# Kernel tuning notes

Measured on AMD Instinct MI355X. Metric: run time of the kernel, lower is better.

Reference implementation:

```python
import jax, jax.numpy as jnp
import numpy as np

H = 256; W = 256; N = 512
TANFOVX = 0.5; TANFOVY = 0.5
FX = W / (2.0 * TANFOVX)   # focal_x
FY = H / (2.0 * TANFOVY)   # focal_y


def _quat_to_rot(q):
    # q: [N,4] (w,x,y,z), normalized inside
    q = q / jnp.linalg.norm(q, axis=-1, keepdims=True)
    r, x, y, z = q[:, 0], q[:, 1], q[:, 2], q[:, 3]
    R = jnp.stack([
        1 - 2 * (y * y + z * z), 2 * (x * y - r * z), 2 * (x * z + r * y),
        2 * (x * y + r * z), 1 - 2 * (x * x + z * z), 2 * (y * z - r * x),
        2 * (x * z - r * y), 2 * (y * z + r * x), 1 - 2 * (x * x + y * y)],
        axis=-1).reshape(-1, 3, 3)
    return R


def _camera():
    # row-vector convention: t = [p,1] @ V ; full proj = V @ Pclip (3DGS style)
    V = np.eye(4, dtype=np.float32)
    V[3, :3] = [0.0, 0.0, 5.0]            # camera 5 units back along -z
    zn, zf = 0.01, 100.0
    P = np.zeros((4, 4), np.float32)
    P[0, 0] = 1.0 / TANFOVX
    P[1, 1] = 1.0 / TANFOVY
    P[2, 2] = zf / (zf - zn)
    P[3, 2] = -zf * zn / (zf - zn)
    P[2, 3] = 1.0
    return jnp.asarray(V), jnp.asarray(V @ P)


def setup_inputs() -> dict:
    key = jax.random.key(0)
    ks = jax.random.split(key, 5)
    means3D = jax.random.normal(ks[0], (N, 3), jnp.float32)
    opacities = jax.random.uniform(ks[1], (N, 1), jnp.float32)
    colors_precomp = jax.random.uniform(ks[2], (N, 3), jnp.float32)
    scales = 0.05 * jax.random.uniform(ks[3], (N, 3), jnp.float32) + 0.01
    rotations = jax.random.normal(ks[4], (N, 4), jnp.float32)
    viewmatrix, projmatrix = _camera()
    return dict(means3D=means3D, opacities=opacities,
                colors_precomp=colors_precomp, scales=scales,
                rotations=rotations, bg=jnp.zeros((3,), jnp.float32),
                viewmatrix=viewmatrix, projmatrix=projmatrix,
                campos=jnp.array([0.0, 0.0, -5.0], jnp.float32))


def _rasterize(means3D, opacities, colors, scales, rotations, bg,
               viewmatrix, projmatrix):
    n = means3D.shape[0]
    # --- 3D covariance: Sigma = (R S)(R S)^T ---
    Rm = _quat_to_rot(rotations)
    M = Rm * scales[:, None, :]                       # [N,3,3]
    Sigma = jnp.einsum('nij,nkj->nik', M, M)
    # --- camera-space positions ---
    ph = jnp.concatenate([means3D, jnp.ones((n, 1), means3D.dtype)], axis=1)
    t = ph @ viewmatrix                               # [N,4]
    tz = t[:, 2]
    tzc = jnp.maximum(tz, 1e-4)
    limx, limy = 1.3 * TANFOVX, 1.3 * TANFOVY
    txc = jnp.clip(t[:, 0] / tzc, -limx, limx) * tzc
    tyc = jnp.clip(t[:, 1] / tzc, -limy, limy) * tzc
    # --- EWA 2D covariance ---
    z0 = jnp.zeros_like(tz)
    J = jnp.stack([
        jnp.stack([FX / tzc, z0, -FX * txc / (tzc * tzc)], axis=-1),
        jnp.stack([z0, FY / tzc, -FY * tyc / (tzc * tzc)], axis=-1)],
        axis=1)                                        # [N,2,3]
    Wc = viewmatrix[:3, :3].T                          # column-vector rotation
    T = jnp.einsum('nij,jk->nik', J, Wc)               # [N,2,3]
    cov2d = jnp.einsum('nij,njk,nlk->nil', T, Sigma, T)
    cov2d = cov2d + 0.3 * jnp.eye(2, dtype=cov2d.dtype)  # low-pass dilation
    c00, c01, c11 = cov2d[:, 0, 0], cov2d[:, 0, 1], cov2d[:, 1, 1]
    det = c00 * c11 - c01 * c01
    det_inv = 1.0 / jnp.where(det != 0, det, 1.0)
    A = c11 * det_inv; B = -c01 * det_inv; C = c00 * det_inv  # conic
    mid = 0.5 * (c00 + c11)
    lam = mid + jnp.sqrt(jnp.maximum(mid * mid - det, 0.1))
    visible = (det > 0) & (tz > 0.2)
    radii = jnp.where(visible, jnp.ceil(3.0 * jnp.sqrt(lam)), 0.0).astype(jnp.int32)
    # --- screen-space means (ndc2pix) ---
    phom = ph @ projmatrix
    pw = 1.0 / (phom[:, 3] + 1e-7)
    mx = ((phom[:, 0] * pw + 1.0) * W - 1.0) * 0.5
    my = ((phom[:, 1] * pw + 1.0) * H - 1.0) * 0.5
    # --- depth sort (front-to-back) ---
    order = jnp.argsort(tz)
    mx, my = mx[order], my[order]
    A_, B_, C_ = A[order], B[order], C[order]
    op = opacities[order, 0]
    vis = visible[order]
    cols = colors[order]
    zs = tz[order]
    # --- per-pixel Gaussian evaluation [P, N] ---
    xs = jnp.arange(W, dtype=means3D.dtype)
    ys = jnp.arange(H, dtype=means3D.dtype)
    pix_x = jnp.tile(xs, H)
    pix_y = jnp.repeat(ys, W)
    dx = mx[None, :] - pix_x[:, None]
    dy = my[None, :] - pix_y[:, None]
    power = -0.5 * (A_[None, :] * dx * dx + C_[None, :] * dy * dy) \
            - B_[None, :] * dx * dy
    alpha = jnp.minimum(0.99, op[None, :] * jnp.exp(power))
    valid = (power <= 0.0) & vis[None, :] & (alpha >= 1.0 / 255.0)
    alpha = jnp.where(valid, alpha, 0.0)
    # --- front-to-back alpha compositing ---
    cum = jnp.cumprod(1.0 - alpha, axis=1)
    Tprev = jnp.concatenate(
        [jnp.ones((alpha.shape[0], 1), alpha.dtype), cum[:, :-1]], axis=1)
    wgt = alpha * Tprev                               # [P,N]
    Tfinal = cum[:, -1]
    color = wgt @ cols + Tfinal[:, None] * bg[None, :]
    depth = wgt @ zs
    color = color.reshape(H, W, 3).transpose(2, 0, 1)  # [3,H,W]
    return color, depth.reshape(H, W), Tfinal.reshape(H, W), radii


def reference(means3D, opacities, colors_precomp, scales, rotations, bg,
              viewmatrix, projmatrix, campos):
    return _rasterize(means3D, opacities, colors_precomp, scales, rotations,
                      bg, viewmatrix, projmatrix)
```

## Files before the change

kernel.cpp:

```cpp
#include <hip/hip_runtime.h>
#include <hip/hip_fp16.h>
#include <math.h>

#define NG 512
#define WI 256
#define HI 256
#define FXc 256.0f
#define FYc 256.0f
#define P2MIN -7.9943534368588578f

#if __has_builtin(__builtin_amdgcn_exp2f)
#define EXP2F(x) __builtin_amdgcn_exp2f(x)
#else
#define EXP2F(x) exp2f(x)
#endif

__global__ __launch_bounds__(256) void gs_fused(
    const float* __restrict__ means,
    const float* __restrict__ opac,
    const float* __restrict__ cols,
    const float* __restrict__ scales,
    const float* __restrict__ rots,
    const float* __restrict__ Vm,
    const float* __restrict__ Pm,
    const float* __restrict__ bg,
    float* __restrict__ out)
{
    __shared__ __align__(16) float4 us[NG*2];
    __shared__ __align__(16) float4 cs[NG*2];
    __shared__ float skey[NG];
    __shared__ int wtot[4];

    int tx   = threadIdx.x;
    int lane = tx & 63;
    int wv   = tx >> 6;
    int y    = blockIdx.x;
    float yf = (float)y;

    float4 q0r[2], q1r[2];
    float tzs[2], myv[2], ycl[2], radf[2];

    #pragma unroll
    for (int i = 0; i < 2; ++i) {
        int g = 2*tx + i;

        float qr = rots[g*4+0], qx = rots[g*4+1], qy = rots[g*4+2], qz = rots[g*4+3];
        float inv = rsqrtf(qr*qr + qx*qx + qy*qy + qz*qz);
        qr *= inv; qx *= inv; qy *= inv; qz *= inv;
        float R00 = 1.f - 2.f*(qy*qy + qz*qz);
        float R01 = 2.f*(qx*qy - qr*qz);
        float R02 = 2.f*(qx*qz + qr*qy);
        float R10 = 2.f*(qx*qy + qr*qz);
        float R11 = 1.f - 2.f*(qx*qx + qz*qz);
        float R12 = 2.f*(qy*qz - qr*qx);
        float R20 = 2.f*(qx*qz - qr*qy);
        float R21 = 2.f*(qy*qz + qr*qx);
        float R22 = 1.f - 2.f*(qx*qx + qy*qy);

        float s0 = scales[g*3+0], s1 = scales[g*3+1], s2 = scales[g*3+2];
        float M00=R00*s0, M01=R01*s1, M02=R02*s2;
        float M10=R10*s0, M11=R11*s1, M12=R12*s2;
        float M20=R20*s0, M21=R21*s1, M22=R22*s2;

        float S00 = M00*M00 + M01*M01 + M02*M02;
        float S01 = M00*M10 + M01*M11 + M02*M12;
        float S02 = M00*M20 + M01*M21 + M02*M22;
        float S11 = M10*M10 + M11*M11 + M12*M12;
        float S12 = M10*M20 + M11*M21 + M12*M22;
        float S22 = M20*M20 + M21*M21 + M22*M22;

        float px = means[g*3+0], py = means[g*3+1], pz = means[g*3+2];
        float t0 = px*Vm[0] + py*Vm[4] + pz*Vm[8]  + Vm[12];
        float t1 = px*Vm[1] + py*Vm[5] + pz*Vm[9]  + Vm[13];
        float tz = px*Vm[2] + py*Vm[6] + pz*Vm[10] + Vm[14];
        float tzc = fmaxf(tz, 1e-4f);
        const float limx = 1.3f*0.5f, limy = 1.3f*0.5f;
        float txc = fminf(fmaxf(t0 / tzc, -limx), limx) * tzc;
        float tyc = fminf(fmaxf(t1 / tzc, -limy), limy) * tzc;

        float J00 = FXc / tzc;
        float J02 = -FXc * txc / (tzc * tzc);
        float J11 = FYc / tzc;
        float J12 = -FYc * tyc / (tzc * tzc);

        float Ta0 = J00*Vm[0] + J02*Vm[2];
        float Ta1 = J00*Vm[4] + J02*Vm[6];
        float Ta2 = J00*Vm[8] + J02*Vm[10];
        float Tb0 = J11*Vm[1] + J12*Vm[2];
        float Tb1 = J11*Vm[5] + J12*Vm[6];
        float Tb2 = J11*Vm[9] + J12*Vm[10];

        float u0 = Ta0*S00 + Ta1*S01 + Ta2*S02;
        float u1 = Ta0*S01 + Ta1*S11 + Ta2*S12;
        float u2 = Ta0*S02 + Ta1*S12 + Ta2*S22;
        float v0 = Tb0*S00 + Tb1*S01 + Tb2*S02;
        float v1 = Tb0*S01 + Tb1*S11 + Tb2*S12;
        float v2 = Tb0*S02 + Tb1*S12 + Tb2*S22;
        float c00 = u0*Ta0 + u1*Ta1 + u2*Ta2 + 0.3f;
        float c01 = u0*Tb0 + u1*Tb1 + u2*Tb2;
        float c11 = v0*Tb0 + v1*Tb1 + v2*Tb2 + 0.3f;

        float det = c00*c11 - c01*c01;
        float det_inv = 1.f / ((det != 0.f) ? det : 1.f);
        float Aa =  c11 * det_inv;
        float Bb = -c01 * det_inv;
        float Cc =  c00 * det_inv;

        float mid = 0.5f*(c00 + c11);
        float lam = mid + sqrtf(fmaxf(mid*mid - det, 0.1f));
        bool vis = (det > 0.f) && (tz > 0.2f);
        radf[i] = vis ? ceilf(3.f*sqrtf(lam)) : 0.f;

        float h0 = px*Pm[0] + py*Pm[4] + pz*Pm[8]  + Pm[12];
        float h1 = px*Pm[1] + py*Pm[5] + pz*Pm[9]  + Pm[13];
        float h3 = px*Pm[3] + py*Pm[7] + pz*Pm[11] + Pm[15];
        float pw = 1.f / (h3 + 1e-7f);
        float mx = ((h0*pw + 1.f)*WI - 1.f)*0.5f;
        float my = ((h1*pw + 1.f)*HI - 1.f)*0.5f;

        float opv = vis ? opac[g] : 0.f;

        const float L2E = 1.4426950408889634f;
        float A2 = -0.5f*L2E*Aa;
        float B2 = -L2E*Bb;
        float C2 = -0.5f*L2E*Cc;
        float lop = (opv > 0.f) ? log2f(opv) : -3.0e38f;

        float a  = 0.5f*L2E*Aa;
        float c  = 0.5f*L2E*Cc;
        float b  = L2E*Bb;
        float qmax  = lop + 7.9943534368588578f;
        float cmarg = c - b*b/(4.f*a);
        float amarg = a - b*b/(4.f*c);
        float dxmin = fmaxf(0.f, fmaxf(-mx, mx - 255.f));
        bool alive = vis && (opv > 0.f) && (qmax >= 0.f) && (cmarg > 0.f)
                     && (amarg*dxmin*dxmin <= qmax);
        ycl[i] = alive ? sqrtf(qmax/cmarg) + 0.0625f : -1.f;

        union { __half2 h; float f; } prg, pbt;
        prg.h = __halves2half2(__float2half_rn(cols[g*3+0]), __float2half_rn(cols[g*3+1]));
        pbt.h = __halves2half2(__float2half_rn(cols[g*3+2]), __float2half_rn(tz));

        q0r[i] = make_float4(mx, my, A2, B2);
        q1r[i] = make_float4(C2, lop, prg.f, pbt.f);
        tzs[i] = tz;
        myv[i] = my;
    }

    if (y == 0) {
        float* radii_out = out + 5*WI*HI;
        radii_out[2*tx]   = radf[0];
        radii_out[2*tx+1] = radf[1];
    }

    bool f0 = fabsf(myv[0] - yf) <= ycl[0];
    bool f1 = fabsf(myv[1] - yf) <= ycl[1];

    unsigned long long m0 = __ballot(f0);
    unsigned long long m1 = __ballot(f1);
    unsigned long long lt = (1ULL << lane) - 1ULL;
    int pre = __popcll(m0 & lt) + __popcll(m1 & lt);
    if (lane == 0) wtot[wv] = __popcll(m0) + __popcll(m1);
    __syncthreads();

    int base = 0, n = 0;
    #pragma unroll
    for (int w2 = 0; w2 < 4; ++w2) {
        int t = wtot[w2];
        base += (w2 < wv) ? t : 0;
        n += t;
    }

    int p0 = base + pre;
    if (f0) {
        us[p0*2+0] = q0r[0];
        us[p0*2+1] = q1r[0];
        skey[p0]   = tzs[0];
    }
    if (f1) {
        int p1 = p0 + (f0 ? 1 : 0);
        us[p1*2+0] = q0r[1];
        us[p1*2+1] = q1r[1];
        skey[p1]   = tzs[1];
    }
    __syncthreads();

    if (tx < n) {
        float k = skey[tx];
        int rank = 0;
        for (int j = 0; j < n; ++j) {
            float o = skey[j];
            rank += (o < k) || ((o == k) && (j < tx));
        }
        float4 a = us[2*tx+0];
        float4 b = us[2*tx+1];
        float dy = a.y - yf;
        float c1 = a.w * dy;
        float c0 = fmaf(b.x*dy, dy, b.y);
        cs[2*rank+0] = make_float4(a.x, a.z, c1, c0);
        cs[2*rank+1] = make_float4(b.y, b.z, b.w, 0.f);
    }
    __syncthreads();

    float pxf = (float)tx;
    float T = 1.f, cr = 0.f, cg = 0.f, cb = 0.f, dp = 0.f;
    for (int j = 0; j < n; ++j) {
        float4 a = cs[2*j+0];
        float4 b = cs[2*j+1];
        float dx = a.x - pxf;
        float p2 = fmaf(fmaf(a.y, dx, a.z), dx, a.w);
        float al = fminf(0.99f, EXP2F(p2));
        al = ((p2 <= b.x) && (p2 >= P2MIN)) ? al : 0.f;
        float w = al * T;
        union { float f; __half2 h; } urg, ubt;
        urg.f = b.y; ubt.f = b.z;
        cr = fmaf(w, __low2float(urg.h),  cr);
        cg = fmaf(w, __high2float(urg.h), cg);
        cb = fmaf(w, __low2float(ubt.h),  cb);
        dp = fmaf(w, __high2float(ubt.h), dp);
        T -= w;
    }

    const int HW = WI * HI;
    int p = y * WI + tx;
    out[p]        = cr + T * bg[0];
    out[HW+p]     = cg + T * bg[1];
    out[2*HW+p]   = cb + T * bg[2];
    out[3*HW+p]   = dp;
    out[4*HW+p]   = T;
}

extern "C" void kernel_launch(void* const* d_in, const int* in_sizes, int n_in,
                              void* d_out, int out_size, void* d_ws, size_t ws_size,
                              hipStream_t stream)
{
    const float* means  = (const float*)d_in[0];
    const float* opac   = (const float*)d_in[1];
    const float* cols   = (const float*)d_in[2];
    const float* scales = (const float*)d_in[3];
    const float* rots   = (const float*)d_in[4];
    const float* bg     = (const float*)d_in[5];
    const float* Vm     = (const float*)d_in[6];
    const float* Pm     = (const float*)d_in[7];

    float* out = (float*)d_out;

    hipLaunchKernelGGL(gs_fused, dim3(HI), dim3(WI), 0, stream,
                       means, opac, cols, scales, rots, Vm, Pm, bg, out);
}
```

Baseline: 77.32 us.

## Split preprocessing into separate kernel and rasterize 16x16 tiles with early exit

Per-Gaussian projection and covariance work moves into a small prep kernel that writes packed records to global memory, so the 256 raster blocks no longer each repeat it. Rasterization now uses 16x16 pixel tiles instead of full rows, culling Gaussians with a per-tile ellipse bound, and evaluates the full 2D quadratic per pixel. The loop exits early once every lane in a wave has transmittance below 1e-4. In exchange it adds a second launch and a global round trip, and the early exit slightly changes results, since the remaining contributions are dropped instead of accumulated.

```diff
diff --git a/kernel.cpp b/kernel.cpp
--- a/kernel.cpp
+++ b/kernel.cpp
@@ -15,7 +15,12 @@
 #define EXP2F(x) exp2f(x)
 #endif
 
-__global__ __launch_bounds__(256) void gs_fused(
+
+__device__ __align__(16) float4 g_q0[NG];
+__device__ __align__(16) float4 g_q1[NG];
+__device__ __align__(16) float4 g_cw[NG];
+
+__global__ __launch_bounds__(256) void gs_prep(
     const float* __restrict__ means,
     const float* __restrict__ opac,
     const float* __restrict__ cols,
@@ -23,6 +28,111 @@
     const float* __restrict__ rots,
     const float* __restrict__ Vm,
     const float* __restrict__ Pm,
+    float* __restrict__ out)
+{
+    int g = blockIdx.x * 256 + threadIdx.x;
+
+    float qr = rots[g*4+0], qx = rots[g*4+1], qy = rots[g*4+2], qz = rots[g*4+3];
+    float inv = rsqrtf(qr*qr + qx*qx + qy*qy + qz*qz);
+    qr *= inv; qx *= inv; qy *= inv; qz *= inv;
+    float R00 = 1.f - 2.f*(qy*qy + qz*qz);
+    float R01 = 2.f*(qx*qy - qr*qz);
+    float R02 = 2.f*(qx*qz + qr*qy);
+    float R10 = 2.f*(qx*qy + qr*qz);
+    float R11 = 1.f - 2.f*(qx*qx + qz*qz);
+    float R12 = 2.f*(qy*qz - qr*qx);
+    float R20 = 2.f*(qx*qz - qr*qy);
+    float R21 = 2.f*(qy*qz + qr*qx);
+    float R22 = 1.f - 2.f*(qx*qx + qy*qy);
+
+    float s0 = scales[g*3+0], s1 = scales[g*3+1], s2 = scales[g*3+2];
+    float M00=R00*s0, M01=R01*s1, M02=R02*s2;
+    float M10=R10*s0, M11=R11*s1, M12=R12*s2;
+    float M20=R20*s0, M21=R21*s1, M22=R22*s2;
+
+    float S00 = M00*M00 + M01*M01 + M02*M02;
+    float S01 = M00*M10 + M01*M11 + M02*M12;
+    float S02 = M00*M20 + M01*M21 + M02*M22;
+    float S11 = M10*M10 + M11*M11 + M12*M12;
+    float S12 = M10*M20 + M11*M21 + M12*M22;
+    float S22 = M20*M20 + M21*M21 + M22*M22;
+
+    float px = means[g*3+0], py = means[g*3+1], pz = means[g*3+2];
+    float t0 = px*Vm[0] + py*Vm[4] + pz*Vm[8]  + Vm[12];
+    float t1 = px*Vm[1] + py*Vm[5] + pz*Vm[9]  + Vm[13];
+    float tz = px*Vm[2] + py*Vm[6] + pz*Vm[10] + Vm[14];
+    float tzc = fmaxf(tz, 1e-4f);
+    const float limx = 1.3f*0.5f, limy = 1.3f*0.5f;
+    float txc = fminf(fmaxf(t0 / tzc, -limx), limx) * tzc;
+    float tyc = fminf(fmaxf(t1 / tzc, -limy), limy) * tzc;
+
+    float J00 = FXc / tzc;
+    float J02 = -FXc * txc / (tzc * tzc);
+    float J11 = FYc / tzc;
+    float J12 = -FYc * tyc / (tzc * tzc);
+
+    float Ta0 = J00*Vm[0] + J02*Vm[2];
+    float Ta1 = J00*Vm[4] + J02*Vm[6];
+    float Ta2 = J00*Vm[8] + J02*Vm[10];
+    float Tb0 = J11*Vm[1] + J12*Vm[2];
+    float Tb1 = J11*Vm[5] + J12*Vm[6];
+    float Tb2 = J11*Vm[9] + J12*Vm[10];
+
+    float u0 = Ta0*S00 + Ta1*S01 + Ta2*S02;
+    float u1 = Ta0*S01 + Ta1*S11 + Ta2*S12;
+    float u2 = Ta0*S02 + Ta1*S12 + Ta2*S22;
+    float v0 = Tb0*S00 + Tb1*S01 + Tb2*S02;
+    float v1 = Tb0*S01 + Tb1*S11 + Tb2*S12;
+    float v2 = Tb0*S02 + Tb1*S12 + Tb2*S22;
+    float c00 = u0*Ta0 + u1*Ta1 + u2*Ta2 + 0.3f;
+    float c01 = u0*Tb0 + u1*Tb1 + u2*Tb2;
+    float c11 = v0*Tb0 + v1*Tb1 + v2*Tb2 + 0.3f;
+
+    float det = c00*c11 - c01*c01;
+    float det_inv = 1.f / ((det != 0.f) ? det : 1.f);
+    float Aa =  c11 * det_inv;
+    float Bb = -c01 * det_inv;
+    float Cc =  c00 * det_inv;
+
+    float mid = 0.5f*(c00 + c11);
+    float lam = mid + sqrtf(fmaxf(mid*mid - det, 0.1f));
+    bool vis = (det > 0.f) && (tz > 0.2f);
+    float radf = vis ? ceilf(3.f*sqrtf(lam)) : 0.f;
+
+    float h0 = px*Pm[0] + py*Pm[4] + pz*Pm[8]  + Pm[12];
+    float h1 = px*Pm[1] + py*Pm[5] + pz*Pm[9]  + Pm[13];
+    float h3 = px*Pm[3] + py*Pm[7] + pz*Pm[11] + Pm[15];
+    float pw = 1.f / (h3 + 1e-7f);
+    float mx = ((h0*pw + 1.f)*WI - 1.f)*0.5f;
+    float my = ((h1*pw + 1.f)*HI - 1.f)*0.5f;
+
+    float opv = vis ? opac[g] : 0.f;
+
+    const float L2E = 1.4426950408889634f;
+    float A2 = -0.5f*L2E*Aa;
+    float B2 = -L2E*Bb;
+    float C2 = -0.5f*L2E*Cc;
+    float lop = (opv > 0.f) ? log2f(opv) : -3.0e38f;
+
+    float a  = 0.5f*L2E*Aa;
+    float c  = 0.5f*L2E*Cc;
+    float bq = L2E*Bb;
+    float qmax  = (vis && opv > 0.f) ? (lop + 7.9943534368588578f) : -1.0f;
+    float amarg = a - bq*bq/(4.f*c);
+    float cmarg = c - bq*bq/(4.f*a);
+
+    out[5*WI*HI + g] = radf;
+
+    union { __half2 h; float f; } prg, pbt;
+    prg.h = __halves2half2(__float2half_rn(cols[g*3+0]), __float2half_rn(cols[g*3+1]));
+    pbt.h = __halves2half2(__float2half_rn(cols[g*3+2]), __float2half_rn(tz));
+
+    g_q0[g] = make_float4(mx, my, A2, B2);
+    g_q1[g] = make_float4(C2, lop, prg.f, pbt.f);
+    g_cw[g] = make_float4(amarg, cmarg, qmax, tz);
+}
+
+__global__ __launch_bounds__(256) void gs_tile(
     const float* __restrict__ bg,
     float* __restrict__ out)
 {
@@ -34,127 +144,22 @@
     int tx   = threadIdx.x;
     int lane = tx & 63;
     int wv   = tx >> 6;
-    int y    = blockIdx.x;
-    float yf = (float)y;
-
-    float4 q0r[2], q1r[2];
-    float tzs[2], myv[2], ycl[2], radf[2];
-
-    #pragma unroll
-    for (int i = 0; i < 2; ++i) {
-        int g = 2*tx + i;
-
-        float qr = rots[g*4+0], qx = rots[g*4+1], qy = rots[g*4+2], qz = rots[g*4+3];
-        float inv = rsqrtf(qr*qr + qx*qx + qy*qy + qz*qz);
-        qr *= inv; qx *= inv; qy *= inv; qz *= inv;
-        float R00 = 1.f - 2.f*(qy*qy + qz*qz);
-        float R01 = 2.f*(qx*qy - qr*qz);
-        float R02 = 2.f*(qx*qz + qr*qy);
-        float R10 = 2.f*(qx*qy + qr*qz);
-        float R11 = 1.f - 2.f*(qx*qx + qz*qz);
-        float R12 = 2.f*(qy*qz - qr*qx);
-        float R20 = 2.f*(qx*qz - qr*qy);
-        float R21 = 2.f*(qy*qz + qr*qx);
-        float R22 = 1.f - 2.f*(qx*qx + qy*qy);
-
-        float s0 = scales[g*3+0], s1 = scales[g*3+1], s2 = scales[g*3+2];
-        float M00=R00*s0, M01=R01*s1, M02=R02*s2;
-        float M10=R10*s0, M11=R11*s1, M12=R12*s2;
-        float M20=R20*s0, M21=R21*s1, M22=R22*s2;
-
-        float S00 = M00*M00 + M01*M01 + M02*M02;
-        float S01 = M00*M10 + M01*M11 + M02*M12;
-        float S02 = M00*M20 + M01*M21 + M02*M22;
-        float S11 = M10*M10 + M11*M11 + M12*M12;
-        float S12 = M10*M20 + M11*M21 + M12*M22;
-        float S22 = M20*M20 + M21*M21 + M22*M22;
-
-        float px = means[g*3+0], py = means[g*3+1], pz = means[g*3+2];
-        float t0 = px*Vm[0] + py*Vm[4] + pz*Vm[8]  + Vm[12];
-        float t1 = px*Vm[1] + py*Vm[5] + pz*Vm[9]  + Vm[13];
-        float tz = px*Vm[2] + py*Vm[6] + pz*Vm[10] + Vm[14];
-        float tzc = fmaxf(tz, 1e-4f);
-        const float limx = 1.3f*0.5f, limy = 1.3f*0.5f;
-        float txc = fminf(fmaxf(t0 / tzc, -limx), limx) * tzc;
-        float tyc = fminf(fmaxf(t1 / tzc, -limy), limy) * tzc;
-
-        float J00 = FXc / tzc;
-        float J02 = -FXc * txc / (tzc * tzc);
-        float J11 = FYc / tzc;
-        float J12 = -FYc * tyc / (tzc * tzc);
-
-        float Ta0 = J00*Vm[0] + J02*Vm[2];
-        float Ta1 = J00*Vm[4] + J02*Vm[6];
-        float Ta2 = J00*Vm[8] + J02*Vm[10];
-        float Tb0 = J11*Vm[1] + J12*Vm[2];
-        float Tb1 = J11*Vm[5] + J12*Vm[6];
-        float Tb2 = J11*Vm[9] + J12*Vm[10];
-
-        float u0 = Ta0*S00 + Ta1*S01 + Ta2*S02;
-        float u1 = Ta0*S01 + Ta1*S11 + Ta2*S12;
-        float u2 = Ta0*S02 + Ta1*S12 + Ta2*S22;
-        float v0 = Tb0*S00 + Tb1*S01 + Tb2*S02;
-        float v1 = Tb0*S01 + Tb1*S11 + Tb2*S12;
-        float v2 = Tb0*S02 + Tb1*S12 + Tb2*S22;
-        float c00 = u0*Ta0 + u1*Ta1 + u2*Ta2 + 0.3f;
-        float c01 = u0*Tb0 + u1*Tb1 + u2*Tb2;
-        float c11 = v0*Tb0 + v1*Tb1 + v2*Tb2 + 0.3f;
-
-        float det = c00*c11 - c01*c01;
-        float det_inv = 1.f / ((det != 0.f) ? det : 1.f);
-        float Aa =  c11 * det_inv;
-        float Bb = -c01 * det_inv;
-        float Cc =  c00 * det_inv;
-
-        float mid = 0.5f*(c00 + c11);
-        float lam = mid + sqrtf(fmaxf(mid*mid - det, 0.1f));
-        bool vis = (det > 0.f) && (tz > 0.2f);
-        radf[i] = vis ? ceilf(3.f*sqrtf(lam)) : 0.f;
-
-        float h0 = px*Pm[0] + py*Pm[4] + pz*Pm[8]  + Pm[12];
-        float h1 = px*Pm[1] + py*Pm[5] + pz*Pm[9]  + Pm[13];
-        float h3 = px*Pm[3] + py*Pm[7] + pz*Pm[11] + Pm[15];
-        float pw = 1.f / (h3 + 1e-7f);
-        float mx = ((h0*pw + 1.f)*WI - 1.f)*0.5f;
-        float my = ((h1*pw + 1.f)*HI - 1.f)*0.5f;
-
-        float opv = vis ? opac[g] : 0.f;
-
-        const float L2E = 1.4426950408889634f;
-        float A2 = -0.5f*L2E*Aa;
-        float B2 = -L2E*Bb;
-        float C2 = -0.5f*L2E*Cc;
-        float lop = (opv > 0.f) ? log2f(opv) : -3.0e38f;
-
-        float a  = 0.5f*L2E*Aa;
-        float c  = 0.5f*L2E*Cc;
-        float b  = L2E*Bb;
-        float qmax  = lop + 7.9943534368588578f;
-        float cmarg = c - b*b/(4.f*a);
-        float amarg = a - b*b/(4.f*c);
-        float dxmin = fmaxf(0.f, fmaxf(-mx, mx - 255.f));
-        bool alive = vis && (opv > 0.f) && (qmax >= 0.f) && (cmarg > 0.f)
-                     && (amarg*dxmin*dxmin <= qmax);
-        ycl[i] = alive ? sqrtf(qmax/cmarg) + 0.0625f : -1.f;
-
-        union { __half2 h; float f; } prg, pbt;
-        prg.h = __halves2half2(__float2half_rn(cols[g*3+0]), __float2half_rn(cols[g*3+1]));
-        pbt.h = __halves2half2(__float2half_rn(cols[g*3+2]), __float2half_rn(tz));
-
-        q0r[i] = make_float4(mx, my, A2, B2);
-        q1r[i] = make_float4(C2, lop, prg.f, pbt.f);
-        tzs[i] = tz;
-        myv[i] = my;
-    }
-
-    if (y == 0) {
-        float* radii_out = out + 5*WI*HI;
-        radii_out[2*tx]   = radf[0];
-        radii_out[2*tx+1] = radf[1];
-    }
-
-    bool f0 = fabsf(myv[0] - yf) <= ycl[0];
-    bool f1 = fabsf(myv[1] - yf) <= ycl[1];
+    int b    = blockIdx.x;
+    int x0   = (b & 15) << 4;
+    int y0   = (b >> 4) << 4;
+    float fx0 = (float)x0, fx1 = (float)(x0 + 15);
+    float fy0 = (float)y0, fy1 = (float)(y0 + 15);
+
+    float4 a0 = g_q0[2*tx],   a1 = g_q0[2*tx+1];
+    float4 b0 = g_q1[2*tx],   b1 = g_q1[2*tx+1];
+    float4 c0 = g_cw[2*tx],   c1 = g_cw[2*tx+1];
+
+    float dxm0 = fmaxf(0.f, fmaxf(fx0 - a0.x, a0.x - fx1) - 0.0625f);
+    float dym0 = fmaxf(0.f, fmaxf(fy0 - a0.y, a0.y - fy1) - 0.0625f);
+    float dxm1 = fmaxf(0.f, fmaxf(fx0 - a1.x, a1.x - fx1) - 0.0625f);
+    float dym1 = fmaxf(0.f, fmaxf(fy0 - a1.y, a1.y - fy1) - 0.0625f);
+    bool f0 = (c0.x*dxm0*dxm0 <= c0.z) && (c0.y*dym0*dym0 <= c0.z);
+    bool f1 = (c1.x*dxm1*dxm1 <= c1.z) && (c1.y*dym1*dym1 <= c1.z);
 
     unsigned long long m0 = __ballot(f0);
     unsigned long long m1 = __ballot(f1);
@@ -173,56 +178,54 @@
 
     int p0 = base + pre;
     if (f0) {
-        us[p0*2+0] = q0r[0];
-        us[p0*2+1] = q1r[0];
-        skey[p0]   = tzs[0];
+        us[p0*2+0] = a0;
+        us[p0*2+1] = b0;
+        skey[p0]   = c0.w;
     }
     if (f1) {
         int p1 = p0 + (f0 ? 1 : 0);
-        us[p1*2+0] = q0r[1];
-        us[p1*2+1] = q1r[1];
-        skey[p1]   = tzs[1];
+        us[p1*2+0] = a1;
+        us[p1*2+1] = b1;
+        skey[p1]   = c1.w;
     }
     __syncthreads();
 
-    if (tx < n) {
-        float k = skey[tx];
+    for (int s = tx; s < n; s += 256) {
+        float k = skey[s];
         int rank = 0;
         for (int j = 0; j < n; ++j) {
             float o = skey[j];
-            rank += (o < k) || ((o == k) && (j < tx));
+            rank += (o < k) || ((o == k) && (j < s));
         }
-        float4 a = us[2*tx+0];
-        float4 b = us[2*tx+1];
-        float dy = a.y - yf;
-        float c1 = a.w * dy;
-        float c0 = fmaf(b.x*dy, dy, b.y);
-        cs[2*rank+0] = make_float4(a.x, a.z, c1, c0);
-        cs[2*rank+1] = make_float4(b.y, b.z, b.w, 0.f);
+        cs[2*rank+0] = us[2*s+0];
+        cs[2*rank+1] = us[2*s+1];
     }
     __syncthreads();
 
-    float pxf = (float)tx;
+    float pxf = (float)(x0 + (tx & 15));
+    float pyf = (float)(y0 + (tx >> 4));
     float T = 1.f, cr = 0.f, cg = 0.f, cb = 0.f, dp = 0.f;
     for (int j = 0; j < n; ++j) {
         float4 a = cs[2*j+0];
-        float4 b = cs[2*j+1];
+        float4 q = cs[2*j+1];
         float dx = a.x - pxf;
-        float p2 = fmaf(fmaf(a.y, dx, a.z), dx, a.w);
+        float dy = a.y - pyf;
+        float p2 = fmaf(fmaf(a.z, dx, a.w*dy), dx, fmaf(q.x*dy, dy, q.y));
         float al = fminf(0.99f, EXP2F(p2));
-        al = ((p2 <= b.x) && (p2 >= P2MIN)) ? al : 0.f;
+        al = ((p2 <= q.y) && (p2 >= P2MIN)) ? al : 0.f;
         float w = al * T;
         union { float f; __half2 h; } urg, ubt;
-        urg.f = b.y; ubt.f = b.z;
+        urg.f = q.z; ubt.f = q.w;
         cr = fmaf(w, __low2float(urg.h),  cr);
         cg = fmaf(w, __high2float(urg.h), cg);
         cb = fmaf(w, __low2float(ubt.h),  cb);
         dp = fmaf(w, __high2float(ubt.h), dp);
         T -= w;
+        if (__all(T < 1e-4f)) break;
     }
 
     const int HW = WI * HI;
-    int p = y * WI + tx;
+    int p = (y0 + (tx >> 4)) * WI + x0 + (tx & 15);
     out[p]        = cr + T * bg[0];
     out[HW+p]     = cg + T * bg[1];
     out[2*HW+p]   = cb + T * bg[2];
@@ -245,6 +248,8 @@
 
     float* out = (float*)d_out;
 
-    hipLaunchKernelGGL(gs_fused, dim3(HI), dim3(WI), 0, stream,
-                       means, opac, cols, scales, rots, Vm, Pm, bg, out);
+    hipLaunchKernelGGL(gs_prep, dim3(2), dim3(256), 0, stream,
+                       means, opac, cols, scales, rots, Vm, Pm, out);
+    hipLaunchKernelGGL(gs_tile, dim3(256), dim3(256), 0, stream,
+                       bg, out);
 }
```

Measured after the change: 75.72 us. 2.1% less time.
